# Performance work log

Hardware: AMD Instinct MI355X
Metric: run time of the kernel (lower is better)

## Reference

```python
import jax, jax.numpy as jnp
import numpy as np

NEG_SLOPE = 0.2  # PyG GATConv default leaky_relu slope
EPS = 1e-16     # PyG softmax denominator epsilon


def gat_conv(x, src, dst, edge_attr, W, att_src, att_dst, W_edge, att_edge, bias):
    """Single-head PyG GATConv with edge_dim. x:[N,Fin] -> [N,Fout].
    src/dst already include self-loops; edge_attr matches their length."""
    N = x.shape[0]
    h = x @ W                      # [N, Fout] transformed node features
    a_s = h @ att_src              # [N] per-node source logit contribution
    a_d = h @ att_dst              # [N]
    a_e = (edge_attr @ W_edge) @ att_edge   # [E] edge contribution
    logits = jax.nn.leaky_relu(a_s[src] + a_d[dst] + a_e, NEG_SLOPE)  # [E]
    # segment softmax over destination nodes
    m = jax.ops.segment_max(logits, dst, num_segments=N)    # [N]
    m = jnp.where(jnp.isfinite(m), m, 0.0)
    e = jnp.exp(logits - m[dst])                             # [E]
    denom = jax.ops.segment_sum(e, dst, num_segments=N)      # [N]
    alpha = e / (denom[dst] + EPS)                            # [E]
    # scatter-aggregate weighted messages
    out = jax.ops.segment_sum(alpha[:, None] * h[src], dst, num_segments=N)
    return out + bias


def setup_inputs() -> dict:
    key = jax.random.key(0)
    ks = jax.random.split(key, 16)
    N, E, F_in, H, C, ED = 100000, 1600000, 128, 64, 2, 1
    inp = {
        "x": jax.random.normal(ks[0], (N, F_in), dtype=jnp.float32),
        "edge_index": jax.random.randint(ks[1], (2, E), 0, N, dtype=jnp.int32),
        "edge_attr": jax.random.normal(ks[2], (E, ED), dtype=jnp.float32),
        # layer 1 params (Glorot-ish scale)
        "W1": jax.random.normal(ks[3], (F_in, H), dtype=jnp.float32) * (1.0 / np.sqrt(F_in)),
        "att_src1": jax.random.normal(ks[4], (H,), dtype=jnp.float32) * (1.0 / np.sqrt(H)),
        "att_dst1": jax.random.normal(ks[5], (H,), dtype=jnp.float32) * (1.0 / np.sqrt(H)),
        "W_edge1": jax.random.normal(ks[6], (ED, H), dtype=jnp.float32),
        "att_edge1": jax.random.normal(ks[7], (H,), dtype=jnp.float32) * (1.0 / np.sqrt(H)),
        "bias1": jnp.zeros((H,), dtype=jnp.float32),
        # layer 2 params
        "W2": jax.random.normal(ks[8], (H, C), dtype=jnp.float32) * (1.0 / np.sqrt(H)),
        "att_src2": jax.random.normal(ks[9], (C,), dtype=jnp.float32),
        "att_dst2": jax.random.normal(ks[10], (C,), dtype=jnp.float32),
        "W_edge2": jax.random.normal(ks[11], (ED, C), dtype=jnp.float32),
        "att_edge2": jax.random.normal(ks[12], (C,), dtype=jnp.float32),
        "bias2": jnp.zeros((C,), dtype=jnp.float32),
    }
    return inp


def reference(x, edge_index, edge_attr,
              W1, att_src1, att_dst1, W_edge1, att_edge1, bias1,
              W2, att_src2, att_dst2, W_edge2, att_edge2, bias2):
    N = x.shape[0]
    # PyG GATConv add_self_loops=True, fill_value='mean' for edge_attr
    loop = jnp.arange(N, dtype=edge_index.dtype)
    src = jnp.concatenate([edge_index[0], loop])
    dst = jnp.concatenate([edge_index[1], loop])
    ea_mean = jnp.mean(edge_attr, axis=0, keepdims=True)              # [1, ED]
    ea = jnp.concatenate([edge_attr, jnp.broadcast_to(ea_mean, (N, edge_attr.shape[1]))])

    h = gat_conv(x, src, dst, ea, W1, att_src1, att_dst1, W_edge1, att_edge1, bias1)
    h = jax.nn.relu(h)  # dropout is identity in eval mode
    out = gat_conv(h, src, dst, ea, W2, att_src2, att_dst2, W_edge2, att_edge2, bias2)
    return jax.nn.log_softmax(out, axis=1)
```

## Files before the change

### kernel.cpp

```cpp
#include <hip/hip_runtime.h>
#include <math.h>

#define NEG_SLOPE 0.2f
#define EPSF 1e-16f

constexpr int FIN = 128;
constexpr int H   = 64;
constexpr int C   = 2;
constexpr int BSHIFT = 8;
constexpr int NBUCK_MAX = 1024;
constexpr int CHUNK = 4096;
constexpr int CAP   = 6144;

typedef short v8s __attribute__((ext_vector_type(8)));
typedef float v4f __attribute__((ext_vector_type(4)));
typedef unsigned short u16;

__device__ inline void split_bf16(float v, u16& hi, u16& lo) {
    unsigned u = __float_as_uint(v);
    unsigned r = (u + 0x7FFFu + ((u >> 16) & 1u)) >> 16;
    hi = (u16)r;
    float hf = __uint_as_float(r << 16);
    float l = v - hf;
    unsigned ul = __float_as_uint(l);
    lo = (u16)((ul + 0x7FFFu + ((ul >> 16) & 1u)) >> 16);
}

__device__ inline u16 to_bf16(float v) {
    unsigned u = __float_as_uint(v);
    return (u16)((u + 0x7FFFu + ((u >> 16) & 1u)) >> 16);
}
__device__ inline float blo(int v) { return __uint_as_float((unsigned)v << 16); }
__device__ inline float bhi(int v) { return __uint_as_float((unsigned)v & 0xFFFF0000u); }

__device__ inline int scan1024_excl(int v, int* wtot, int t) {
    int lane = t & 63, w = t >> 6;
    int incl = v;
    #pragma unroll
    for (int o = 1; o < 64; o <<= 1) {
        int u = __shfl_up(incl, o, 64);
        if (lane >= o) incl += u;
    }
    if (lane == 63) wtot[w] = incl;
    __syncthreads();
    int woff = 0;
    for (int i = 0; i < w; i++) woff += wtot[i];
    return woff + incl - v;
}

__global__ __launch_bounds__(1024) void pre_kernel(const float* __restrict__ ea,
                                                   const int* __restrict__ dst, int E,
                                                   float* __restrict__ csum, int* __restrict__ cnt,
                                                   const float* __restrict__ W1,
                                                   u16* __restrict__ Wt_hi, u16* __restrict__ Wt_lo,
                                                   int NBUCK) {
    int c = blockIdx.x, t = threadIdx.x;
    int gid = c * 1024 + t;
    if (gid < FIN * H) {
        int k = gid >> 6, f = gid & 63;
        u16 h, l;
        split_bf16(W1[gid], h, l);
        int idx = ((k >> 3) << 9) + (f << 3) + (k & 7);
        Wt_hi[idx] = h;
        Wt_lo[idx] = l;
    }
    __shared__ int lh[NBUCK_MAX];
    __shared__ float wsum[16];
    lh[t] = 0;
    __syncthreads();
    int base = c * CHUNK;
    int cntE = min(CHUNK, E - base);
    float acc = 0.f;
    for (int i = t; i < cntE; i += 1024) {
        int e = base + i;
        acc += ea[e];
        atomicAdd(&lh[dst[e] >> BSHIFT], 1);
    }
    for (int off = 32; off; off >>= 1) acc += __shfl_down(acc, off, 64);
    int lane = t & 63, wv = t >> 6;
    if (lane == 0) wsum[wv] = acc;
    __syncthreads();
    if (t == 0) {
        float s = 0.f;
        #pragma unroll
        for (int i = 0; i < 16; i++) s += wsum[i];
        csum[c] = s;
    }
    if (t < NBUCK) cnt[(size_t)c * NBUCK + t] = lh[t];
}

__global__ __launch_bounds__(256) void soff_kernel(const int* __restrict__ cnt,
                                                   int NBUCK, int NCHUNK,
                                                   int* __restrict__ bcount, int* __restrict__ poff,
                                                   const float* __restrict__ csum, int E,
                                                   const float* __restrict__ W_edge1,
                                                   const float* __restrict__ att_edge1,
                                                   const float* __restrict__ W_edge2,
                                                   const float* __restrict__ att_edge2,
                                                   float* __restrict__ scal,
                                                   int* __restrict__ rowN) {
    int b = blockIdx.x, t = threadIdx.x;
    int per = (NCHUNK + 255) / 256;
    int v[8];
    int s = 0;
    for (int j = 0; j < per; j++) {
        int c = t * per + j;
        v[j] = (c < NCHUNK) ? cnt[(size_t)c * NBUCK + b] : 0;
        s += v[j];
    }
    __shared__ int red[256];
    __shared__ float ws4[4];
    red[t] = s;
    __syncthreads();
    for (int off = 1; off < 256; off <<= 1) {
        int u = (t >= off) ? red[t - off] : 0;
        __syncthreads();
        red[t] += u;
        __syncthreads();
    }
    int run = red[t] - s;
    for (int j = 0; j < per; j++) {
        int c = t * per + j;
        if (c < NCHUNK) poff[(size_t)b * NCHUNK + c] = run;
        run += v[j];
    }
    if (t == 255) bcount[b] = red[255];
    if (b == 0) {
        float acc = 0.f;
        for (int i = t; i < NCHUNK; i += 256) acc += csum[i];
        for (int off = 32; off; off >>= 1) acc += __shfl_down(acc, off, 64);
        if ((t & 63) == 0) ws4[t >> 6] = acc;
        __syncthreads();
        if (t == 0) {
            float tot = ws4[0] + ws4[1] + ws4[2] + ws4[3];
            float c1 = 0.f;
            for (int i = 0; i < H; i++) c1 += W_edge1[i] * att_edge1[i];
            float c2 = 0.f;
            for (int i = 0; i < C; i++) c2 += W_edge2[i] * att_edge2[i];
            scal[0] = tot / (float)E; scal[1] = c1; scal[2] = c2;
            *rowN = E;
        }
    }
}

__global__ __launch_bounds__(1024) void stage_kernel(
        const int* __restrict__ src, const int* __restrict__ dst, const float* __restrict__ ea,
        int E, const int* __restrict__ cnt, const int* __restrict__ poff,
        const int* __restrict__ bcount,
        int2* __restrict__ staging, int* __restrict__ bbase_out, int NBUCK, int NCHUNK) {
    __shared__ int   bb[NBUCK_MAX];
    __shared__ int   cur[NBUCK_MAX];
    __shared__ int   gofs[NBUCK_MAX];
    __shared__ int2  sbuf[CHUNK];
    __shared__ short sbkt[CHUNK];
    __shared__ int   wt16[16];
    int t = threadIdx.x;
    int c = blockIdx.x;
    int base = c * CHUNK;
    int cntE = min(CHUNK, E - base);
    int bv = (t < NBUCK) ? bcount[t] : 0;
    int bx = scan1024_excl(bv, wt16, t);
    if (t < NBUCK) bb[t] = bx;
    if (c == 0) {
        if (t < NBUCK) bbase_out[t] = bx;
        if (t == 0) bbase_out[NBUCK] = E;
    }
    __syncthreads();
    int h = (t < NBUCK) ? cnt[(size_t)c * NBUCK + t] : 0;
    int p = scan1024_excl(h, wt16, t);
    if (t < NBUCK) {
        if (h) gofs[t] = bb[t] + poff[(size_t)t * NCHUNK + c] - p;
        cur[t] = p;
    }
    __syncthreads();
    for (int i = t; i < cntE; i += 1024) {
        int e = base + i;
        int d = dst[e];
        int b = d >> BSHIFT;
        int slot = atomicAdd(&cur[b], 1);
        sbuf[slot] = make_int2(src[e] | ((d & ((1 << BSHIFT) - 1)) << 20), __float_as_int(ea[e]));
        sbkt[slot] = (short)b;
    }
    __syncthreads();
    for (int j = t; j < cntE; j += 1024)
        staging[gofs[sbkt[j]] + j] = sbuf[j];
}

__global__ __launch_bounds__(256) void gemm1_mfma_kernel(
        const float* __restrict__ x,
        const u16* __restrict__ Wt_hi, const u16* __restrict__ Wt_lo,
        const float* __restrict__ att_src, const float* __restrict__ att_dst,
        u16* __restrict__ h1b, float* __restrict__ a_s, float* __restrict__ a_d, int N) {
    __shared__ u16 WhL[FIN * H];
    __shared__ u16 WlL[FIN * H];
    int t = threadIdx.x;
    int w = t >> 6, lane = t & 63;
    int m = lane & 15, q = lane >> 4;
    int base = blockIdx.x * 64 + w * 16;
    int nodeA = base + m;
    bool inA = nodeA < N;
    const float* xrow = x + (size_t)nodeA * FIN;

    float4 fh[4], fl4[4];
    {
        const float4* gh = (const float4*)Wt_hi;
        const float4* gl = (const float4*)Wt_lo;
        #pragma unroll
        for (int i = 0; i < 4; i++) {
            fh[i]  = gh[t + i * 256];
            fl4[i] = gl[t + i * 256];
        }
    }
    float4 xv4[8];
    #pragma unroll
    for (int kt = 0; kt < 4; kt++) {
        if (inA) {
            const float4* p = (const float4*)(xrow + kt * 32 + q * 8);
            xv4[kt * 2]     = p[0];
            xv4[kt * 2 + 1] = p[1];
        } else {
            xv4[kt * 2]     = make_float4(0.f, 0.f, 0.f, 0.f);
            xv4[kt * 2 + 1] = make_float4(0.f, 0.f, 0.f, 0.f);
        }
    }
    {
        float4* sh = (float4*)WhL;
        float4* sl = (float4*)WlL;
        #pragma unroll
        for (int i = 0; i < 4; i++) {
            sh[t + i * 256] = fh[i];
            sl[t + i * 256] = fl4[i];
        }
    }

    v8s ah[4], al[4];
    #pragma unroll
    for (int kt = 0; kt < 4; kt++) {
        float xv[8];
        xv[0] = xv4[kt * 2].x;     xv[1] = xv4[kt * 2].y;
        xv[2] = xv4[kt * 2].z;     xv[3] = xv4[kt * 2].w;
        xv[4] = xv4[kt * 2 + 1].x; xv[5] = xv4[kt * 2 + 1].y;
        xv[6] = xv4[kt * 2 + 1].z; xv[7] = xv4[kt * 2 + 1].w;
        #pragma unroll
        for (int j = 0; j < 8; j++) {
            u16 hb, lb;
            split_bf16(xv[j], hb, lb);
            ah[kt][j] = (short)hb;
            al[kt][j] = (short)lb;
        }
    }
    __syncthreads();

    float ps[4] = {0.f, 0.f, 0.f, 0.f};
    float pd[4] = {0.f, 0.f, 0.f, 0.f};
    #pragma unroll
    for (int ft = 0; ft < 4; ft++) {
        v4f acc = {0.f, 0.f, 0.f, 0.f};
        #pragma unroll
        for (int kt = 0; kt < 4; kt++) {
            int fi = ((kt * 4 + q) << 9) + ((ft * 16 + m) << 3);
            v8s bh = *(const v8s*)(WhL + fi);
            v8s bl = *(const v8s*)(WlL + fi);
            acc = __builtin_amdgcn_mfma_f32_16x16x32_bf16(ah[kt], bh, acc, 0, 0, 0);
            acc = __builtin_amdgcn_mfma_f32_16x16x32_bf16(al[kt], bh, acc, 0, 0, 0);
            acc = __builtin_amdgcn_mfma_f32_16x16x32_bf16(ah[kt], bl, acc, 0, 0, 0);
        }
        int f = ft * 16 + m;
        float asf = att_src[f], adf = att_dst[f];
        #pragma unroll
        for (int r = 0; r < 4; r++) {
            int node = base + q * 4 + r;
            if (node < N) h1b[(size_t)node * H + f] = to_bf16(acc[r]);
            ps[r] += acc[r] * asf;
            pd[r] += acc[r] * adf;
        }
    }
    #pragma unroll
    for (int msk = 1; msk < 16; msk <<= 1) {
        #pragma unroll
        for (int r = 0; r < 4; r++) {
            ps[r] += __shfl_xor(ps[r], msk, 64);
            pd[r] += __shfl_xor(pd[r], msk, 64);
        }
    }
    if (m == 0) {
        #pragma unroll
        for (int r = 0; r < 4; r++) {
            int node = base + q * 4 + r;
            if (node < N) { a_s[node] = ps[r]; a_d[node] = pd[r]; }
        }
    }
}

__global__ __launch_bounds__(1024) void bfin_kernel(
        const int2* __restrict__ staging, const int* __restrict__ bbase,
        const float* __restrict__ scal,
        const float* __restrict__ a_s1, const float* __restrict__ a_d1,
        int* __restrict__ row, int2* __restrict__ sedge, float* __restrict__ sea2, int N) {
    __shared__ int   nh[256];
    __shared__ int   wt16[16];
    __shared__ int2  ebuf[CAP];
    __shared__ float abuf[CAP];
    int b = blockIdx.x, t = threadIdx.x;
    int beg = bbase[b], end = bbase[b + 1];
    int cnt = end - beg;
    int node0 = b << BSHIFT;
    float c1 = scal[1];
    if (t < 256) nh[t] = 0;
    __syncthreads();
    for (int i = beg + t; i < end; i += 1024)
        atomicAdd(&nh[(unsigned)staging[i].x >> 20], 1);
    __syncthreads();
    int v = (t < 256) ? nh[t] : 0;
    int lane = t & 63, w = t >> 6;
    int incl = v;
    #pragma unroll
    for (int o = 1; o < 64; o <<= 1) {
        int u = __shfl_up(incl, o, 64);
        if (lane >= o) incl += u;
    }
    if (w < 4 && lane == 63) wt16[w] = incl;
    __syncthreads();
    int woff = 0;
    int wl = w < 4 ? w : 4;
    for (int i = 0; i < wl; i++) woff += wt16[i];
    int excl = woff + incl - v;
    int node = node0 + t;
    if (t < 256 && node < N) row[node] = beg + excl;
    bool fast = (cnt <= CAP);
    if (t < 256) nh[t] = fast ? excl : beg + excl;
    __syncthreads();
    for (int i = beg + t; i < end; i += 1024) {
        int2 r = staging[i];
        int dlow = (unsigned)r.x >> 20;
        int sn = r.x & 0xFFFFF;
        float eav = __int_as_float(r.y);
        float lg = a_s1[sn] + a_d1[node0 + dlow] + eav * c1;
        lg = lg > 0.f ? lg : NEG_SLOPE * lg;
        float ex = __expf(lg);
        int pos = atomicAdd(&nh[dlow], 1);
        if (fast) {
            ebuf[pos] = make_int2(sn, __float_as_int(ex));
            abuf[pos] = eav;
        } else {
            sedge[pos] = make_int2(sn, __float_as_int(ex));
            sea2[pos] = eav;
        }
    }
    __syncthreads();
    if (fast) {
        for (int j = t; j < cnt; j += 1024) {
            sedge[beg + j] = ebuf[j];
            sea2[beg + j]  = abuf[j];
        }
    }
}

__global__ __launch_bounds__(256) void agg1_kernel(
        const int* __restrict__ row, const int2* __restrict__ sedge,
        const float* __restrict__ scal,
        const float* __restrict__ a_s, const float* __restrict__ a_d,
        const u16* __restrict__ h1b,
        const float* __restrict__ bias1, const float* __restrict__ W2,
        const float* __restrict__ att_src2, const float* __restrict__ att_dst2,
        float* __restrict__ h2, float* __restrict__ a_s2, float* __restrict__ a_d2,
        int N) {
    int wv = threadIdx.x >> 6;
    int lane = threadIdx.x & 63;
    int g  = lane >> 3;
    int fl = lane & 7;
    int n = blockIdx.x * 32 + wv * 8 + g;
    if (n >= N) return;
    int beg = row[n], end = row[n + 1];
    float den = 0.f;
    float acc[8] = {0.f, 0.f, 0.f, 0.f, 0.f, 0.f, 0.f, 0.f};
    const u16* hrow = h1b + fl * 8;
    int i = beg;
    for (; i + 2 <= end; i += 2) {
        int2 e0 = sedge[i], e1 = sedge[i + 1];
        int4 h0 = *(const int4*)(hrow + (size_t)e0.x * H);
        int4 h1v = *(const int4*)(hrow + (size_t)e1.x * H);
        float x0 = __int_as_float(e0.y), x1 = __int_as_float(e1.y);
        den += x0 + x1;
        acc[0] += x0 * blo(h0.x); acc[1] += x0 * bhi(h0.x);
        acc[2] += x0 * blo(h0.y); acc[3] += x0 * bhi(h0.y);
        acc[4] += x0 * blo(h0.z); acc[5] += x0 * bhi(h0.z);
        acc[6] += x0 * blo(h0.w); acc[7] += x0 * bhi(h0.w);
        acc[0] += x1 * blo(h1v.x); acc[1] += x1 * bhi(h1v.x);
        acc[2] += x1 * blo(h1v.y); acc[3] += x1 * bhi(h1v.y);
        acc[4] += x1 * blo(h1v.z); acc[5] += x1 * bhi(h1v.z);
        acc[6] += x1 * blo(h1v.w); acc[7] += x1 * bhi(h1v.w);
    }
    if (i < end) {
        int2 e0 = sedge[i];
        int4 h0 = *(const int4*)(hrow + (size_t)e0.x * H);
        float x0 = __int_as_float(e0.y);
        den += x0;
        acc[0] += x0 * blo(h0.x); acc[1] += x0 * bhi(h0.x);
        acc[2] += x0 * blo(h0.y); acc[3] += x0 * bhi(h0.y);
        acc[4] += x0 * blo(h0.z); acc[5] += x0 * bhi(h0.z);
        acc[6] += x0 * blo(h0.w); acc[7] += x0 * bhi(h0.w);
    }
    {
        float lg = a_s[n] + a_d[n] + scal[0] * scal[1];
        lg = lg > 0.f ? lg : NEG_SLOPE * lg;
        float ex = __expf(lg);
        int4 hs = *(const int4*)(hrow + (size_t)n * H);
        den += ex;
        acc[0] += ex * blo(hs.x); acc[1] += ex * bhi(hs.x);
        acc[2] += ex * blo(hs.y); acc[3] += ex * bhi(hs.y);
        acc[4] += ex * blo(hs.z); acc[5] += ex * bhi(hs.z);
        acc[6] += ex * blo(hs.w); acc[7] += ex * bhi(hs.w);
    }
    float inv = 1.f / (den + EPSF);
    float p0 = 0.f, p1 = 0.f;
    #pragma unroll
    for (int k = 0; k < 8; k++) {
        int f = fl * 8 + k;
        float hr = acc[k] * inv + bias1[f];
        hr = fmaxf(hr, 0.f);
        p0 += hr * W2[f * C + 0];
        p1 += hr * W2[f * C + 1];
    }
    #pragma unroll
    for (int msk = 1; msk < 8; msk <<= 1) {
        p0 += __shfl_xor(p0, msk, 64);
        p1 += __shfl_xor(p1, msk, 64);
    }
    if (fl == 0) {
        h2[(size_t)n * C + 0] = p0;
        h2[(size_t)n * C + 1] = p1;
        a_s2[n] = p0 * att_src2[0] + p1 * att_src2[1];
        a_d2[n] = p0 * att_dst2[0] + p1 * att_dst2[1];
    }
}

__global__ __launch_bounds__(256) void agg2_kernel(
        const int* __restrict__ row, const int2* __restrict__ sedge, const float* __restrict__ sea2,
        const float* __restrict__ scal,
        const float* __restrict__ a_s2, const float* __restrict__ a_d2,
        const float* __restrict__ h2, const float* __restrict__ bias2,
        float* __restrict__ out, int N) {
    int wv = threadIdx.x >> 6;
    int lane = threadIdx.x & 63;
    int g  = lane >> 3;
    int fl = lane & 7;
    int n = blockIdx.x * 32 + wv * 8 + g;
    if (n >= N) return;
    float c2 = scal[2];
    float ad = a_d2[n];
    int beg = row[n], end = row[n + 1];
    float den = 0.f, m0 = 0.f, m1 = 0.f;
    for (int i = beg + fl; i < end; i += 8) {
        int s = sedge[i].x;
        float lg = a_s2[s] + ad + sea2[i] * c2;
        lg = lg > 0.f ? lg : NEG_SLOPE * lg;
        float ex = __expf(lg);
        den += ex;
        m0 += ex * h2[(size_t)s * C + 0];
        m1 += ex * h2[(size_t)s * C + 1];
    }
    if (fl == 0) {
        float lg = a_s2[n] + ad + scal[0] * c2;
        lg = lg > 0.f ? lg : NEG_SLOPE * lg;
        float ex = __expf(lg);
        den += ex;
        m0 += ex * h2[(size_t)n * C + 0];
        m1 += ex * h2[(size_t)n * C + 1];
    }
    #pragma unroll
    for (int msk = 1; msk < 8; msk <<= 1) {
        den += __shfl_xor(den, msk, 64);
        m0  += __shfl_xor(m0, msk, 64);
        m1  += __shfl_xor(m1, msk, 64);
    }
    if (fl == 0) {
        float dn = den + EPSF;
        float o0 = m0 / dn + bias2[0];
        float o1 = m1 / dn + bias2[1];
        float mx = fmaxf(o0, o1);
        float lse = mx + logf(expf(o0 - mx) + expf(o1 - mx));
        out[(size_t)n * C + 0] = o0 - lse;
        out[(size_t)n * C + 1] = o1 - lse;
    }
}

extern "C" void kernel_launch(void* const* d_in, const int* in_sizes, int n_in,
                              void* d_out, int out_size, void* d_ws, size_t ws_size,
                              hipStream_t stream) {
    const float* x        = (const float*)d_in[0];
    const int*   ei       = (const int*)d_in[1];
    const float* ea       = (const float*)d_in[2];
    const float* W1       = (const float*)d_in[3];
    const float* att_src1 = (const float*)d_in[4];
    const float* att_dst1 = (const float*)d_in[5];
    const float* W_edge1  = (const float*)d_in[6];
    const float* att_edge1= (const float*)d_in[7];
    const float* bias1    = (const float*)d_in[8];
    const float* W2       = (const float*)d_in[9];
    const float* att_src2 = (const float*)d_in[10];
    const float* att_dst2 = (const float*)d_in[11];
    const float* W_edge2  = (const float*)d_in[12];
    const float* att_edge2= (const float*)d_in[13];
    const float* bias2    = (const float*)d_in[14];

    const int N  = in_sizes[0] / FIN;
    const int E  = in_sizes[1] / 2;
    const int* srcp = ei;
    const int* dstp = ei + E;
    const int NBUCK  = (N + (1 << BSHIFT) - 1) >> BSHIFT;
    const int NCHUNK = (E + CHUNK - 1) / CHUNK;

    char* wsb = (char*)d_ws;
    size_t off = 0;
    auto alloc = [&](size_t bytes) { void* p = wsb + off; off += (bytes + 255) & ~size_t(255); return p; };
    float* csum   = (float*)alloc((size_t)2048 * 4);
    int*   bcount = (int*)alloc((size_t)NBUCK_MAX * 4);
    int*   bbase  = (int*)alloc((size_t)(NBUCK_MAX + 1) * 4);
    int*   cnt    = (int*)alloc((size_t)NCHUNK * NBUCK * 4);
    int*   poff   = (int*)alloc((size_t)NBUCK * NCHUNK * 4);
    int*   row    = (int*)alloc((size_t)(N + 1) * 4);
    int2*  sedge  = (int2*)alloc((size_t)(E + 8) * 8);
    float* sea2   = (float*)alloc((size_t)E * 4);
    int2*  staging= (int2*)alloc((size_t)E * 8);
    u16*   h1b    = (u16*)alloc((size_t)N * H * 2);
    u16*   Wt_hi  = (u16*)alloc((size_t)FIN * H * 2);
    u16*   Wt_lo  = (u16*)alloc((size_t)FIN * H * 2);
    float* a_s1   = (float*)alloc((size_t)N * 4);
    float* a_d1   = (float*)alloc((size_t)N * 4);
    float* h2     = (float*)alloc((size_t)N * C * 4);
    float* a_s2   = (float*)alloc((size_t)N * 4);
    float* a_d2   = (float*)alloc((size_t)N * 4);
    float* scal   = (float*)alloc(3 * 4);

    pre_kernel<<<NCHUNK, 1024, 0, stream>>>(ea, dstp, E, csum, cnt, W1, Wt_hi, Wt_lo, NBUCK);
    soff_kernel<<<NBUCK, 256, 0, stream>>>(cnt, NBUCK, NCHUNK, bcount, poff,
                                           csum, E, W_edge1, att_edge1, W_edge2, att_edge2,
                                           scal, row + N);
    stage_kernel<<<NCHUNK, 1024, 0, stream>>>(srcp, dstp, ea, E, cnt, poff, bcount,
                                              staging, bbase, NBUCK, NCHUNK);
    gemm1_mfma_kernel<<<(N + 63) / 64, 256, 0, stream>>>(x, Wt_hi, Wt_lo, att_src1, att_dst1,
                                                         h1b, a_s1, a_d1, N);
    bfin_kernel<<<NBUCK, 1024, 0, stream>>>(staging, bbase, scal, a_s1, a_d1, row, sedge, sea2, N);
    agg1_kernel<<<(N + 31) / 32, 256, 0, stream>>>(row, sedge, scal, a_s1, a_d1, h1b,
                                                   bias1, W2, att_src2, att_dst2,
                                                   h2, a_s2, a_d2, N);
    agg2_kernel<<<(N + 31) / 32, 256, 0, stream>>>(row, sedge, sea2, scal, a_s2, a_d2, h2, bias2,
                                                   (float*)d_out, N);
}
```

Measured before the change: 216.4 us.

## Fuse histogram with GEMM1, replace offset scan with atomics, unroll aggregation

Merges the edge histogram and the first GEMM into one heterogeneous launch, so histogram blocks and GEMM blocks can run concurrently. Each GEMM block now converts W1 to split bf16 in shared memory on its own, and GEMM blocks grow to 256 nodes. The separate per-bucket scan kernel is removed: bucket totals come from global atomics, and per-chunk offsets are claimed with atomicAdd on a zeroed cursor. That makes edge order within a bucket nondeterministic. The agg1 edge loop is unrolled to four gathers per iteration to raise memory-level parallelism.

```diff
diff --git a/kernel.cpp b/kernel.cpp
--- a/kernel.cpp
+++ b/kernel.cpp
@@ -48,169 +48,58 @@
     return woff + incl - v;
 }
 
-__global__ __launch_bounds__(1024) void pre_kernel(const float* __restrict__ ea,
-                                                   const int* __restrict__ dst, int E,
-                                                   float* __restrict__ csum, int* __restrict__ cnt,
-                                                   const float* __restrict__ W1,
-                                                   u16* __restrict__ Wt_hi, u16* __restrict__ Wt_lo,
-                                                   int NBUCK) {
-    int c = blockIdx.x, t = threadIdx.x;
-    int gid = c * 1024 + t;
-    if (gid < FIN * H) {
-        int k = gid >> 6, f = gid & 63;
-        u16 h, l;
-        split_bf16(W1[gid], h, l);
-        int idx = ((k >> 3) << 9) + (f << 3) + (k & 7);
-        Wt_hi[idx] = h;
-        Wt_lo[idx] = l;
-    }
-    __shared__ int lh[NBUCK_MAX];
-    __shared__ float wsum[16];
-    lh[t] = 0;
-    __syncthreads();
-    int base = c * CHUNK;
-    int cntE = min(CHUNK, E - base);
-    float acc = 0.f;
-    for (int i = t; i < cntE; i += 1024) {
-        int e = base + i;
-        acc += ea[e];
-        atomicAdd(&lh[dst[e] >> BSHIFT], 1);
-    }
-    for (int off = 32; off; off >>= 1) acc += __shfl_down(acc, off, 64);
-    int lane = t & 63, wv = t >> 6;
-    if (lane == 0) wsum[wv] = acc;
-    __syncthreads();
-    if (t == 0) {
-        float s = 0.f;
-        #pragma unroll
-        for (int i = 0; i < 16; i++) s += wsum[i];
-        csum[c] = s;
-    }
-    if (t < NBUCK) cnt[(size_t)c * NBUCK + t] = lh[t];
-}
-
-__global__ __launch_bounds__(256) void soff_kernel(const int* __restrict__ cnt,
-                                                   int NBUCK, int NCHUNK,
-                                                   int* __restrict__ bcount, int* __restrict__ poff,
-                                                   const float* __restrict__ csum, int E,
-                                                   const float* __restrict__ W_edge1,
-                                                   const float* __restrict__ att_edge1,
-                                                   const float* __restrict__ W_edge2,
-                                                   const float* __restrict__ att_edge2,
-                                                   float* __restrict__ scal,
-                                                   int* __restrict__ rowN) {
-    int b = blockIdx.x, t = threadIdx.x;
-    int per = (NCHUNK + 255) / 256;
-    int v[8];
-    int s = 0;
-    for (int j = 0; j < per; j++) {
-        int c = t * per + j;
-        v[j] = (c < NCHUNK) ? cnt[(size_t)c * NBUCK + b] : 0;
-        s += v[j];
-    }
-    __shared__ int red[256];
-    __shared__ float ws4[4];
-    red[t] = s;
-    __syncthreads();
-    for (int off = 1; off < 256; off <<= 1) {
-        int u = (t >= off) ? red[t - off] : 0;
+__global__ __launch_bounds__(1024) void fused_pre_gemm_kernel(
+        const float* __restrict__ ea, const int* __restrict__ dst, int E,
+        float* __restrict__ csum, int* __restrict__ cnt, int* __restrict__ bcount,
+        const float* __restrict__ x, const float* __restrict__ W1,
+        const float* __restrict__ att_src, const float* __restrict__ att_dst,
+        u16* __restrict__ h1b, float* __restrict__ a_s, float* __restrict__ a_d,
+        int N, int NBUCK, int NCHUNK) {
+    int t = threadIdx.x;
+    if ((int)blockIdx.x < NCHUNK) {
+        __shared__ int lh[NBUCK_MAX];
+        __shared__ float wsum[16];
+        int c = blockIdx.x;
+        lh[t] = 0;
         __syncthreads();
-        red[t] += u;
-        __syncthreads();
-    }
-    int run = red[t] - s;
-    for (int j = 0; j < per; j++) {
-        int c = t * per + j;
-        if (c < NCHUNK) poff[(size_t)b * NCHUNK + c] = run;
-        run += v[j];
-    }
-    if (t == 255) bcount[b] = red[255];
-    if (b == 0) {
+        int base = c * CHUNK;
+        int cntE = min(CHUNK, E - base);
         float acc = 0.f;
-        for (int i = t; i < NCHUNK; i += 256) acc += csum[i];
+        for (int i = t; i < cntE; i += 1024) {
+            int e = base + i;
+            acc += ea[e];
+            atomicAdd(&lh[dst[e] >> BSHIFT], 1);
+        }
         for (int off = 32; off; off >>= 1) acc += __shfl_down(acc, off, 64);
-        if ((t & 63) == 0) ws4[t >> 6] = acc;
+        int lane = t & 63, wv = t >> 6;
+        if (lane == 0) wsum[wv] = acc;
         __syncthreads();
         if (t == 0) {
-            float tot = ws4[0] + ws4[1] + ws4[2] + ws4[3];
-            float c1 = 0.f;
-            for (int i = 0; i < H; i++) c1 += W_edge1[i] * att_edge1[i];
-            float c2 = 0.f;
-            for (int i = 0; i < C; i++) c2 += W_edge2[i] * att_edge2[i];
-            scal[0] = tot / (float)E; scal[1] = c1; scal[2] = c2;
-            *rowN = E;
-        }
-    }
-}
-
-__global__ __launch_bounds__(1024) void stage_kernel(
-        const int* __restrict__ src, const int* __restrict__ dst, const float* __restrict__ ea,
-        int E, const int* __restrict__ cnt, const int* __restrict__ poff,
-        const int* __restrict__ bcount,
-        int2* __restrict__ staging, int* __restrict__ bbase_out, int NBUCK, int NCHUNK) {
-    __shared__ int   bb[NBUCK_MAX];
-    __shared__ int   cur[NBUCK_MAX];
-    __shared__ int   gofs[NBUCK_MAX];
-    __shared__ int2  sbuf[CHUNK];
-    __shared__ short sbkt[CHUNK];
-    __shared__ int   wt16[16];
-    int t = threadIdx.x;
-    int c = blockIdx.x;
-    int base = c * CHUNK;
-    int cntE = min(CHUNK, E - base);
-    int bv = (t < NBUCK) ? bcount[t] : 0;
-    int bx = scan1024_excl(bv, wt16, t);
-    if (t < NBUCK) bb[t] = bx;
-    if (c == 0) {
-        if (t < NBUCK) bbase_out[t] = bx;
-        if (t == 0) bbase_out[NBUCK] = E;
-    }
-    __syncthreads();
-    int h = (t < NBUCK) ? cnt[(size_t)c * NBUCK + t] : 0;
-    int p = scan1024_excl(h, wt16, t);
-    if (t < NBUCK) {
-        if (h) gofs[t] = bb[t] + poff[(size_t)t * NCHUNK + c] - p;
-        cur[t] = p;
-    }
-    __syncthreads();
-    for (int i = t; i < cntE; i += 1024) {
-        int e = base + i;
-        int d = dst[e];
-        int b = d >> BSHIFT;
-        int slot = atomicAdd(&cur[b], 1);
-        sbuf[slot] = make_int2(src[e] | ((d & ((1 << BSHIFT) - 1)) << 20), __float_as_int(ea[e]));
-        sbkt[slot] = (short)b;
-    }
-    __syncthreads();
-    for (int j = t; j < cntE; j += 1024)
-        staging[gofs[sbkt[j]] + j] = sbuf[j];
-}
-
-__global__ __launch_bounds__(256) void gemm1_mfma_kernel(
-        const float* __restrict__ x,
-        const u16* __restrict__ Wt_hi, const u16* __restrict__ Wt_lo,
-        const float* __restrict__ att_src, const float* __restrict__ att_dst,
-        u16* __restrict__ h1b, float* __restrict__ a_s, float* __restrict__ a_d, int N) {
+            float s = 0.f;
+            #pragma unroll
+            for (int i = 0; i < 16; i++) s += wsum[i];
+            csum[c] = s;
+        }
+        if (t < NBUCK) {
+            int v = lh[t];
+            cnt[(size_t)c * NBUCK + t] = v;
+            if (v) atomicAdd(&bcount[t], v);
+        }
+        return;
+    }
     __shared__ u16 WhL[FIN * H];
     __shared__ u16 WlL[FIN * H];
-    int t = threadIdx.x;
+    int bid = blockIdx.x - NCHUNK;
     int w = t >> 6, lane = t & 63;
     int m = lane & 15, q = lane >> 4;
-    int base = blockIdx.x * 64 + w * 16;
+    int base = bid * 256 + w * 16;
     int nodeA = base + m;
     bool inA = nodeA < N;
     const float* xrow = x + (size_t)nodeA * FIN;
 
-    float4 fh[4], fl4[4];
-    {
-        const float4* gh = (const float4*)Wt_hi;
-        const float4* gl = (const float4*)Wt_lo;
-        #pragma unroll
-        for (int i = 0; i < 4; i++) {
-            fh[i]  = gh[t + i * 256];
-            fl4[i] = gl[t + i * 256];
-        }
-    }
+    float w1v[8];
+    #pragma unroll
+    for (int j = 0; j < 8; j++) w1v[j] = W1[t + j * 1024];
     float4 xv4[8];
     #pragma unroll
     for (int kt = 0; kt < 4; kt++) {
@@ -223,16 +112,16 @@
             xv4[kt * 2 + 1] = make_float4(0.f, 0.f, 0.f, 0.f);
         }
     }
-    {
-        float4* sh = (float4*)WhL;
-        float4* sl = (float4*)WlL;
-        #pragma unroll
-        for (int i = 0; i < 4; i++) {
-            sh[t + i * 256] = fh[i];
-            sl[t + i * 256] = fl4[i];
-        }
-    }
-
+    #pragma unroll
+    for (int j = 0; j < 8; j++) {
+        int gid = t + j * 1024;
+        int k = gid >> 6, f = gid & 63;
+        u16 hb, lb;
+        split_bf16(w1v[j], hb, lb);
+        int idx = ((k >> 3) << 9) + (f << 3) + (k & 7);
+        WhL[idx] = hb;
+        WlL[idx] = lb;
+    }
     v8s ah[4], al[4];
     #pragma unroll
     for (int kt = 0; kt < 4; kt++) {
@@ -290,6 +179,68 @@
             if (node < N) { a_s[node] = ps[r]; a_d[node] = pd[r]; }
         }
     }
+}
+
+__global__ __launch_bounds__(1024) void stage_kernel(
+        const int* __restrict__ src, const int* __restrict__ dst, const float* __restrict__ ea,
+        int E, const int* __restrict__ cnt, const int* __restrict__ bcount,
+        int* __restrict__ gcur,
+        int2* __restrict__ staging, int* __restrict__ bbase_out, int NBUCK, int NCHUNK,
+        const float* __restrict__ csum,
+        const float* __restrict__ W_edge1, const float* __restrict__ att_edge1,
+        const float* __restrict__ W_edge2, const float* __restrict__ att_edge2,
+        float* __restrict__ scal, int* __restrict__ rowN) {
+    __shared__ int   bb[NBUCK_MAX];
+    __shared__ int   cur[NBUCK_MAX];
+    __shared__ int   gofs[NBUCK_MAX];
+    __shared__ int2  sbuf[CHUNK];
+    __shared__ short sbkt[CHUNK];
+    __shared__ int   wt16[16];
+    __shared__ float ws16[16];
+    int t = threadIdx.x;
+    int c = blockIdx.x;
+    int base = c * CHUNK;
+    int cntE = min(CHUNK, E - base);
+    int bv = (t < NBUCK) ? bcount[t] : 0;
+    int bx = scan1024_excl(bv, wt16, t);
+    if (t < NBUCK) bb[t] = bx;
+    if (c == 0) {
+        if (t < NBUCK) bbase_out[t] = bx;
+        if (t == 0) { bbase_out[NBUCK] = E; *rowN = E; }
+        float acc = 0.f;
+        for (int i = t; i < NCHUNK; i += 1024) acc += csum[i];
+        for (int off = 32; off; off >>= 1) acc += __shfl_down(acc, off, 64);
+        if ((t & 63) == 0) ws16[t >> 6] = acc;
+    }
+    __syncthreads();
+    if (c == 0 && t == 0) {
+        float tot = 0.f;
+        #pragma unroll
+        for (int i = 0; i < 16; i++) tot += ws16[i];
+        float c1 = 0.f;
+        for (int i = 0; i < H; i++) c1 += W_edge1[i] * att_edge1[i];
+        float c2 = 0.f;
+        for (int i = 0; i < C; i++) c2 += W_edge2[i] * att_edge2[i];
+        scal[0] = tot / (float)E; scal[1] = c1; scal[2] = c2;
+    }
+    int h = (t < NBUCK) ? cnt[(size_t)c * NBUCK + t] : 0;
+    int p = scan1024_excl(h, wt16, t);
+    if (t < NBUCK) {
+        if (h) gofs[t] = bb[t] + atomicAdd(&gcur[t], h) - p;
+        cur[t] = p;
+    }
+    __syncthreads();
+    for (int i = t; i < cntE; i += 1024) {
+        int e = base + i;
+        int d = dst[e];
+        int b = d >> BSHIFT;
+        int slot = atomicAdd(&cur[b], 1);
+        sbuf[slot] = make_int2(src[e] | ((d & ((1 << BSHIFT) - 1)) << 20), __float_as_int(ea[e]));
+        sbkt[slot] = (short)b;
+    }
+    __syncthreads();
+    for (int j = t; j < cntE; j += 1024)
+        staging[gofs[sbkt[j]] + j] = sbuf[j];
 }
 
 __global__ __launch_bounds__(1024) void bfin_kernel(
@@ -354,6 +305,14 @@
             sea2[beg + j]  = abuf[j];
         }
     }
+}
+
+__device__ inline void accum8(float acc[8], float& den, float xw, int4 hv) {
+    den += xw;
+    acc[0] += xw * blo(hv.x); acc[1] += xw * bhi(hv.x);
+    acc[2] += xw * blo(hv.y); acc[3] += xw * bhi(hv.y);
+    acc[4] += xw * blo(hv.z); acc[5] += xw * bhi(hv.z);
+    acc[6] += xw * blo(hv.w); acc[7] += xw * bhi(hv.w);
 }
 
 __global__ __launch_bounds__(256) void agg1_kernel(
@@ -376,41 +335,36 @@
     float acc[8] = {0.f, 0.f, 0.f, 0.f, 0.f, 0.f, 0.f, 0.f};
     const u16* hrow = h1b + fl * 8;
     int i = beg;
-    for (; i + 2 <= end; i += 2) {
+    for (; i + 4 <= end; i += 4) {
+        int2 e0 = sedge[i], e1 = sedge[i + 1], e2 = sedge[i + 2], e3 = sedge[i + 3];
+        int4 h0 = *(const int4*)(hrow + (size_t)e0.x * H);
+        int4 h1v = *(const int4*)(hrow + (size_t)e1.x * H);
+        int4 h2v = *(const int4*)(hrow + (size_t)e2.x * H);
+        int4 h3v = *(const int4*)(hrow + (size_t)e3.x * H);
+        accum8(acc, den, __int_as_float(e0.y), h0);
+        accum8(acc, den, __int_as_float(e1.y), h1v);
+        accum8(acc, den, __int_as_float(e2.y), h2v);
+        accum8(acc, den, __int_as_float(e3.y), h3v);
+    }
+    if (i + 2 <= end) {
         int2 e0 = sedge[i], e1 = sedge[i + 1];
         int4 h0 = *(const int4*)(hrow + (size_t)e0.x * H);
         int4 h1v = *(const int4*)(hrow + (size_t)e1.x * H);
-        float x0 = __int_as_float(e0.y), x1 = __int_as_float(e1.y);
-        den += x0 + x1;
-        acc[0] += x0 * blo(h0.x); acc[1] += x0 * bhi(h0.x);
-        acc[2] += x0 * blo(h0.y); acc[3] += x0 * bhi(h0.y);
-        acc[4] += x0 * blo(h0.z); acc[5] += x0 * bhi(h0.z);
-        acc[6] += x0 * blo(h0.w); acc[7] += x0 * bhi(h0.w);
-        acc[0] += x1 * blo(h1v.x); acc[1] += x1 * bhi(h1v.x);
-        acc[2] += x1 * blo(h1v.y); acc[3] += x1 * bhi(h1v.y);
-        acc[4] += x1 * blo(h1v.z); acc[5] += x1 * bhi(h1v.z);
-        acc[6] += x1 * blo(h1v.w); acc[7] += x1 * bhi(h1v.w);
+        accum8(acc, den, __int_as_float(e0.y), h0);
+        accum8(acc, den, __int_as_float(e1.y), h1v);
+        i += 2;
     }
     if (i < end) {
         int2 e0 = sedge[i];
         int4 h0 = *(const int4*)(hrow + (size_t)e0.x * H);
-        float x0 = __int_as_float(e0.y);
-        den += x0;
-        acc[0] += x0 * blo(h0.x); acc[1] += x0 * bhi(h0.x);
-        acc[2] += x0 * blo(h0.y); acc[3] += x0 * bhi(h0.y);
-        acc[4] += x0 * blo(h0.z); acc[5] += x0 * bhi(h0.z);
-        acc[6] += x0 * blo(h0.w); acc[7] += x0 * bhi(h0.w);
+        accum8(acc, den, __int_as_float(e0.y), h0);
     }
     {
         float lg = a_s[n] + a_d[n] + scal[0] * scal[1];
         lg = lg > 0.f ? lg : NEG_SLOPE * lg;
         float ex = __expf(lg);
         int4 hs = *(const int4*)(hrow + (size_t)n * H);
-        den += ex;
-        acc[0] += ex * blo(hs.x); acc[1] += ex * bhi(hs.x);
-        acc[2] += ex * blo(hs.y); acc[3] += ex * bhi(hs.y);
-        acc[4] += ex * blo(hs.z); acc[5] += ex * bhi(hs.z);
-        acc[6] += ex * blo(hs.w); acc[7] += ex * bhi(hs.w);
+        accum8(acc, den, ex, hs);
     }
     float inv = 1.f / (den + EPSF);
     float p0 = 0.f, p1 = 0.f;
@@ -510,22 +464,22 @@
     const int* dstp = ei + E;
     const int NBUCK  = (N + (1 << BSHIFT) - 1) >> BSHIFT;
     const int NCHUNK = (E + CHUNK - 1) / CHUNK;
+    const int NGEMM  = (N + 255) / 256;
 
     char* wsb = (char*)d_ws;
     size_t off = 0;
     auto alloc = [&](size_t bytes) { void* p = wsb + off; off += (bytes + 255) & ~size_t(255); return p; };
+    int*   bcount = (int*)alloc((size_t)NBUCK_MAX * 4);
+    int*   gcur   = (int*)alloc((size_t)NBUCK_MAX * 4);
+    size_t zbytes = off;
     float* csum   = (float*)alloc((size_t)2048 * 4);
-    int*   bcount = (int*)alloc((size_t)NBUCK_MAX * 4);
     int*   bbase  = (int*)alloc((size_t)(NBUCK_MAX + 1) * 4);
     int*   cnt    = (int*)alloc((size_t)NCHUNK * NBUCK * 4);
-    int*   poff   = (int*)alloc((size_t)NBUCK * NCHUNK * 4);
     int*   row    = (int*)alloc((size_t)(N + 1) * 4);
     int2*  sedge  = (int2*)alloc((size_t)(E + 8) * 8);
     float* sea2   = (float*)alloc((size_t)E * 4);
     int2*  staging= (int2*)alloc((size_t)E * 8);
     u16*   h1b    = (u16*)alloc((size_t)N * H * 2);
-    u16*   Wt_hi  = (u16*)alloc((size_t)FIN * H * 2);
-    u16*   Wt_lo  = (u16*)alloc((size_t)FIN * H * 2);
     float* a_s1   = (float*)alloc((size_t)N * 4);
     float* a_d1   = (float*)alloc((size_t)N * 4);
     float* h2     = (float*)alloc((size_t)N * C * 4);
@@ -533,14 +487,14 @@
     float* a_d2   = (float*)alloc((size_t)N * 4);
     float* scal   = (float*)alloc(3 * 4);
 
-    pre_kernel<<<NCHUNK, 1024, 0, stream>>>(ea, dstp, E, csum, cnt, W1, Wt_hi, Wt_lo, NBUCK);
-    soff_kernel<<<NBUCK, 256, 0, stream>>>(cnt, NBUCK, NCHUNK, bcount, poff,
-                                           csum, E, W_edge1, att_edge1, W_edge2, att_edge2,
-                                           scal, row + N);
-    stage_kernel<<<NCHUNK, 1024, 0, stream>>>(srcp, dstp, ea, E, cnt, poff, bcount,
-                                              staging, bbase, NBUCK, NCHUNK);
-    gemm1_mfma_kernel<<<(N + 63) / 64, 256, 0, stream>>>(x, Wt_hi, Wt_lo, att_src1, att_dst1,
-                                                         h1b, a_s1, a_d1, N);
+    hipMemsetAsync(d_ws, 0, zbytes, stream);
+
+    fused_pre_gemm_kernel<<<NCHUNK + NGEMM, 1024, 0, stream>>>(
+        ea, dstp, E, csum, cnt, bcount,
+        x, W1, att_src1, att_dst1, h1b, a_s1, a_d1, N, NBUCK, NCHUNK);
+    stage_kernel<<<NCHUNK, 1024, 0, stream>>>(
+        srcp, dstp, ea, E, cnt, bcount, gcur, staging, bbase, NBUCK, NCHUNK,
+        csum, W_edge1, att_edge1, W_edge2, att_edge2, scal, row + N);
     bfin_kernel<<<NBUCK, 1024, 0, stream>>>(staging, bbase, scal, a_s1, a_d1, row, sedge, sea2, N);
     agg1_kernel<<<(N + 31) / 32, 256, 0, stream>>>(row, sedge, scal, a_s1, a_d1, h1b,
                                                    bias1, W2, att_src2, att_dst2,
```

After: 226.8 us. +4.8%, slower.
